# Optimization experiments

Measured on AMD Instinct MI355X. Metric: run time of the kernel, lower is better.

Reference implementation:

```python
import jax, jax.numpy as jnp
import numpy as np

B, C, H, W = 8, 128, 64, 64

def conv2d(x, w, b, pad):
    # x: [B,C,H,W], w: [O,I,kh,kw] -> NCHW conv with symmetric padding
    y = jax.lax.conv_general_dilated(
        x, w, window_strides=(1, 1), padding=[(pad, pad), (pad, pad)],
        dimension_numbers=("NCHW", "OIHW", "NCHW"))
    return y + b[None, :, None, None]

def setup_inputs() -> dict:
    key = jax.random.key(0)
    ks = jax.random.split(key, 5)
    s3 = 1.0 / np.sqrt(C * 9)  # kaiming-uniform-ish scale for 3x3 conv
    s1 = 1.0 / np.sqrt(C)
    return {
        "x": jax.random.normal(ks[0], (B, C, H, W), jnp.float32),
        "Wq": jax.random.normal(ks[1], (C, C, 3, 3), jnp.float32) * s3,
        "bq": jnp.zeros((C,), jnp.float32),
        "Wk": jax.random.normal(ks[2], (C, C, 3, 3), jnp.float32) * s3,
        "bk": jnp.zeros((C,), jnp.float32),
        "Wv": jax.random.normal(ks[3], (C, C, 3, 3), jnp.float32) * s3,
        "bv": jnp.zeros((C,), jnp.float32),
        "Wo": jax.random.normal(ks[4], (C, C, 1, 1), jnp.float32) * s1,
        "bo": jnp.zeros((C,), jnp.float32),
    }

def reference(x, Wq, bq, Wk, bk, Wv, bv, Wo, bo):
    b, c, h, w = x.shape
    n = h * w
    scale = c ** (-0.5)
    # NOTE: original module defines self.norm but never applies it in forward.
    q = conv2d(x, Wq, bq, 1).reshape(b, c, n)
    k = conv2d(x, Wk, bk, 1).reshape(b, c, n)
    v = conv2d(x, Wv, bv, 1).reshape(b, c, n)
    attn = jax.nn.softmax(jnp.einsum("bci,bcj->bij", q, k) * scale, axis=2)  # [b,n,n]
    out = jnp.einsum("bij,bcj->bci", attn, v).reshape(b, c, h, w)
    out = conv2d(out, Wo, bo, 0)
    return x + out
```

## Files before the change

kernel.cpp:

```cpp
#include <hip/hip_runtime.h>

typedef __attribute__((ext_vector_type(8))) short bf16x8;
typedef __attribute__((ext_vector_type(4))) float f32x4;
typedef __attribute__((ext_vector_type(16))) float f32x16;

static __device__ __forceinline__ unsigned short f2bf(float f) {
    union { float f; unsigned int u; } v; v.f = f;
    unsigned int r = v.u + 0x7FFFu + ((v.u >> 16) & 1u);
    return (unsigned short)(r >> 16);
}

static __device__ __forceinline__ unsigned cvtpk_bf16(float lo, float hi) {
    unsigned r;
    asm("v_cvt_pk_bf16_f32 %0, %1, %2" : "=v"(r) : "v"(lo), "v"(hi));
    return r;
}

#define NRW (27 * 16384)

__global__ __launch_bounds__(256) void repack_k(const float* __restrict__ Wq, const float* __restrict__ Wk,
                                                const float* __restrict__ Wv, const float* __restrict__ Wo,
                                                unsigned short* __restrict__ RW, unsigned short* __restrict__ WoB) {
    int t = blockIdx.x * 256 + threadIdx.x;
    if (t < NRW) {
        int s = t & 7, o = (t >> 3) & 127, g = (t >> 10) & 3, cc = (t >> 12) & 3, tap = t >> 14;
        int conv = tap / 9, kk = tap % 9, kh = kk / 3, kw = kk % 3;
        int c = cc * 32 + g * 8 + s;
        const float* W = (conv == 0) ? Wq : ((conv == 1) ? Wk : Wv);
        RW[t] = f2bf(W[((o * 128 + c) * 3 + kh) * 3 + kw]);
    } else {
        int u = t - NRW;
        if (u < 16384) WoB[u] = f2bf(Wo[u]);
    }
}

__global__ __launch_bounds__(256) void qkv_conv_k(const float* __restrict__ x, const unsigned short* __restrict__ RW,
                                                  const float* __restrict__ bq, const float* __restrict__ bk,
                                                  const float* __restrict__ bv,
                                                  unsigned short* __restrict__ q_ws, unsigned short* __restrict__ k_ws,
                                                  unsigned short* __restrict__ v_ws) {
    __shared__ unsigned short xs[3 * 66 * 128];
    const int tid = threadIdx.x;
    const int b = blockIdx.x >> 6, h = blockIdx.x & 63;
    for (int i = tid; i < 3 * 66 * 128; i += 256) xs[i] = 0;
    __syncthreads();
    for (int ch = tid; ch < 3 * 128 * 16; ch += 256) {
        int r3 = ch >> 11, rem = ch & 2047, c = rem >> 4, w4 = rem & 15;
        int hh = h - 1 + r3;
        if (hh >= 0 && hh < 64) {
            float4 v = *(const float4*)(x + ((b * 128 + c) * 64 + hh) * 64 + w4 * 4);
            float vv[4] = {v.x, v.y, v.z, v.w};
#pragma unroll
            for (int j = 0; j < 4; ++j) {
                int wr = w4 * 4 + j + 1;
                unsigned int byte = (unsigned int)(((r3 * 66 + wr) * 128 + c) * 2) ^ ((wr & 7) << 4);
                *(unsigned short*)((char*)xs + byte) = f2bf(vv[j]);
            }
        }
    }
    __syncthreads();
    const int lane = tid & 63, wave = tid >> 6;
    const int l15 = lane & 15, g = lane >> 4;
    f32x4 acc[4][6];
#pragma unroll
    for (int i = 0; i < 4; ++i)
#pragma unroll
        for (int j = 0; j < 6; ++j) acc[i][j] = (f32x4){0.f, 0.f, 0.f, 0.f};
#pragma unroll 1
    for (int kk = 0; kk < 9; ++kk) {
        const int kw = kk % 3;
#pragma unroll 2
        for (int cc = 0; cc < 4; ++cc) {
            bf16x8 a[4];
#pragma unroll
            for (int mf = 0; mf < 4; ++mf) {
                int wr = mf * 16 + l15 + kw;
                unsigned int byte = (unsigned int)((((kk / 3) * 66 + wr) * 128 + cc * 32 + g * 8) * 2) ^ ((wr & 7) << 4);
                a[mf] = *(const bf16x8*)((const char*)xs + byte);
            }
#pragma unroll
            for (int n6 = 0; n6 < 6; ++n6) {
                int nt = wave * 6 + n6;
                int conv = nt >> 3;
                int o = (nt * 16 + l15) & 127;
                bf16x8 bfr = *(const bf16x8*)(RW + ((((conv * 9 + kk) * 4 + cc) * 4 + g) * 128 + o) * 8);
#pragma unroll
                for (int mf = 0; mf < 4; ++mf)
                    acc[mf][n6] = __builtin_amdgcn_mfma_f32_16x16x32_bf16(a[mf], bfr, acc[mf][n6], 0, 0, 0);
            }
        }
    }
    const float SCALE = 0.08838834764831845f;
#pragma unroll
    for (int n6 = 0; n6 < 6; ++n6) {
        int nt = wave * 6 + n6;
        int conv = nt >> 3;
        int o = (nt * 16 + l15) & 127;
        float bias = (conv == 0) ? bq[o] : ((conv == 1) ? bk[o] : bv[o]);
#pragma unroll
        for (int mf = 0; mf < 4; ++mf) {
#pragma unroll
            for (int r = 0; r < 4; ++r) {
                int pos = h * 64 + mf * 16 + g * 4 + r;
                float val = acc[mf][n6][r] + bias;
                if (conv == 0)      q_ws[(b * 4096 + pos) * 128 + o] = f2bf(val * SCALE);
                else if (conv == 1) k_ws[(b * 4096 + pos) * 128 + o] = f2bf(val);
                else                v_ws[(b * 128 + o) * 4096 + pos] = f2bf(val);
            }
        }
    }
}

#define AS1C(p) ((const __attribute__((address_space(1))) void*)(p))
#define AS3(p)  ((__attribute__((address_space(3))) void*)(p))

__global__ __launch_bounds__(256, 2) void attn_k(
    const unsigned short* __restrict__ q_ws, const unsigned short* __restrict__ k_ws,
    const unsigned short* __restrict__ v_ws, const unsigned short* __restrict__ WoB,
    const float* __restrict__ bo, const float* __restrict__ x, float* __restrict__ out) {
    __shared__ __align__(16) char smem[66560];

    const int tid = threadIdx.x;
    const int lane = tid & 63, wave = tid >> 6;
    const int wj = wave & 1, wi = wave >> 1;
    const int l31 = lane & 31, h = lane >> 5;
    const int b = blockIdx.x & 7;
    const int qt = blockIdx.x >> 3;
    const int ibase = qt * 64;

    const char* kB = (const char*)(k_ws + (size_t)b * 4096 * 128);
    const char* vB = (const char*)(v_ws + (size_t)b * 128 * 4096);

    auto stage = [&](int buf, int kt) {
        char* Kn = smem + buf * 32768;
        char* Vn = Kn + 16384;
#pragma unroll
        for (int q = 0; q < 4; ++q) {
            int slot = (wave * 4 + q) * 64 + lane;
            int krow = slot >> 4, ks = slot & 15;
            int kcs = ks ^ (krow & 15);
            __builtin_amdgcn_global_load_lds(AS1C(kB + (size_t)(kt * 64 + krow) * 256 + kcs * 16),
                                             AS3(Kn + slot * 16), 16, 0, 0);
            int vrow = slot >> 3, vs = slot & 7;
            int vcs = vs ^ (vrow & 7);
            __builtin_amdgcn_global_load_lds(AS1C(vB + (size_t)vrow * 8192 + kt * 128 + vcs * 16),
                                             AS3(Vn + slot * 16), 16, 0, 0);
        }
    };

    stage(0, 0);

    bf16x8 qf[8];
    {
        const unsigned short* qrow = q_ws + ((size_t)b * 4096 + ibase + wi * 32 + l31) * 128;
#pragma unroll
        for (int cc = 0; cc < 8; ++cc) qf[cc] = *(const bf16x8*)(qrow + cc * 16 + h * 8);
    }

    f32x16 oac[4];
#pragma unroll
    for (int cf = 0; cf < 4; ++cf)
#pragma unroll
        for (int r = 0; r < 16; ++r) oac[cf][r] = 0.f;
    float m = -1e30f, ssum = 0.f;

    __syncthreads();

#pragma unroll 1
    for (int kt = 0; kt < 64; ++kt) {
        const int cur = kt & 1;
        const char* Kc = smem + cur * 32768;
        const char* Vc = Kc + 16384;
        if (kt < 63) stage(cur ^ 1, kt + 1);

        f32x16 st;
#pragma unroll
        for (int r = 0; r < 16; ++r) st[r] = 0.f;
        const int jrow = wj * 32 + l31;
        __builtin_amdgcn_s_setprio(1);
#pragma unroll
        for (int cc = 0; cc < 8; ++cc) {
            unsigned byte = (unsigned)(jrow * 256 + (((cc * 2 + h) ^ (jrow & 15)) << 4));
            bf16x8 kf = *(const bf16x8*)(Kc + byte);
            st = __builtin_amdgcn_mfma_f32_32x32x16_bf16(kf, qf[cc], st, 0, 0, 0);
        }
        __builtin_amdgcn_s_setprio(0);

        float tmax = st[0];
#pragma unroll
        for (int r = 1; r < 16; ++r) tmax = fmaxf(tmax, st[r]);
        tmax = fmaxf(tmax, __shfl_xor(tmax, 32));
        if (!__all(tmax <= m)) {
            float mnew = fmaxf(m, tmax);
            float corr = __expf(m - mnew);
            ssum *= corr;
#pragma unroll
            for (int cf = 0; cf < 4; ++cf)
#pragma unroll
                for (int r = 0; r < 16; ++r) oac[cf][r] *= corr;
            m = mnew;
        }

        float ps = 0.f;
        bf16x8 pa[2];
#pragma unroll
        for (int js = 0; js < 2; ++js) {
            float pA0 = __expf(st[8 * js + 0] - m);
            float pA1 = __expf(st[8 * js + 1] - m);
            float pA2 = __expf(st[8 * js + 2] - m);
            float pA3 = __expf(st[8 * js + 3] - m);
            float pB0 = __expf(st[8 * js + 4] - m);
            float pB1 = __expf(st[8 * js + 5] - m);
            float pB2 = __expf(st[8 * js + 6] - m);
            float pB3 = __expf(st[8 * js + 7] - m);
            ps += ((pA0 + pA1) + (pA2 + pA3)) + ((pB0 + pB1) + (pB2 + pB3));
            unsigned a0 = cvtpk_bf16(pA0, pA1), a1 = cvtpk_bf16(pA2, pA3);
            unsigned b0 = cvtpk_bf16(pB0, pB1), b1 = cvtpk_bf16(pB2, pB3);
            auto r0 = __builtin_amdgcn_permlane32_swap(a0, b0, false, false);
            auto r1 = __builtin_amdgcn_permlane32_swap(a1, b1, false, false);
            union { unsigned w[4]; bf16x8 v; } pu;
            pu.w[0] = r0[0];
            pu.w[1] = r1[0];
            pu.w[2] = r0[1];
            pu.w[3] = r1[1];
            pa[js] = pu.v;
        }
        ps += __shfl_xor(ps, 32);
        ssum += ps;

        __builtin_amdgcn_s_setprio(1);
#pragma unroll
        for (int js = 0; js < 2; ++js) {
            const int chunk = wj * 4 + js * 2 + h;
#pragma unroll
            for (int cf = 0; cf < 4; ++cf) {
                int crow = cf * 32 + l31;
                unsigned vbyte = (unsigned)(crow * 128 + ((chunk ^ (crow & 7)) << 4));
                bf16x8 va = *(const bf16x8*)(Vc + vbyte);
                oac[cf] = __builtin_amdgcn_mfma_f32_32x32x16_bf16(va, pa[js], oac[cf], 0, 0, 0);
            }
        }
        __builtin_amdgcn_s_setprio(0);
        __syncthreads();
    }

    float* sRed = (float*)(smem + 65536);
    const int it = wi * 32 + l31;
    if (h == 0) {
        sRed[(wj * 64 + it) * 2] = m;
        sRed[(wj * 64 + it) * 2 + 1] = ssum;
    }
    __syncthreads();
    float m1 = sRed[((wj ^ 1) * 64 + it) * 2];
    float s1 = sRed[((wj ^ 1) * 64 + it) * 2 + 1];
    float M = fmaxf(m, m1);
    float aS = __expf(m - M);
    float inv = 1.0f / (aS * ssum + __expf(m1 - M) * s1);

    char* sBig = smem + 32768;
    if (wj == 1) {
#pragma unroll
        for (int cf = 0; cf < 4; ++cf)
#pragma unroll
            for (int g = 0; g < 4; ++g) {
                int c = cf * 32 + g * 8 + 4 * h;
                f32x4 v4;
#pragma unroll
                for (int k = 0; k < 4; ++k) v4[k] = aS * oac[cf][4 * g + k];
                unsigned byte = (unsigned)(it * 512 + c * 4) ^ ((it & 7) << 4);
                *(f32x4*)(sBig + byte) = v4;
            }
    }
    __syncthreads();
    unsigned short* sOut = (unsigned short*)smem;
    if (wj == 0) {
#pragma unroll
        for (int cf = 0; cf < 4; ++cf)
#pragma unroll
            for (int g = 0; g < 4; ++g) {
                int c = cf * 32 + g * 8 + 4 * h;
                unsigned rbyte = (unsigned)(it * 512 + c * 4) ^ ((it & 7) << 4);
                f32x4 rd = *(const f32x4*)((const char*)sBig + rbyte);
                float u0 = (aS * oac[cf][4 * g + 0] + rd[0]) * inv;
                float u1 = (aS * oac[cf][4 * g + 1] + rd[1]) * inv;
                float u2 = (aS * oac[cf][4 * g + 2] + rd[2]) * inv;
                float u3 = (aS * oac[cf][4 * g + 3] + rd[3]) * inv;
                uint2 pk;
                pk.x = cvtpk_bf16(u0, u1);
                pk.y = cvtpk_bf16(u2, u3);
                unsigned wbyte = (unsigned)(it * 256 + c * 2) ^ ((it & 15) << 4);
                *(uint2*)((char*)sOut + wbyte) = pk;
            }
    }
    __syncthreads();

#pragma unroll
    for (int t = 0; t < 2; ++t) {
        int tt = wave * 2 + t;
        int of = tt >> 1, ifl = tt & 1;
        int ir = ifl * 32 + l31;
        f32x16 acc;
#pragma unroll
        for (int r = 0; r < 16; ++r) acc[r] = 0.f;
#pragma unroll
        for (int cc = 0; cc < 8; ++cc) {
            unsigned bbyte = (unsigned)(ir * 256 + cc * 32 + h * 16) ^ ((ir & 15) << 4);
            bf16x8 bfr = *(const bf16x8*)((const char*)sOut + bbyte);
            bf16x8 wa = *(const bf16x8*)(WoB + (of * 32 + l31) * 128 + cc * 16 + h * 8);
            acc = __builtin_amdgcn_mfma_f32_32x32x16_bf16(wa, bfr, acc, 0, 0, 0);
        }
        int iglob = ibase + ir;
#pragma unroll
        for (int r = 0; r < 16; ++r) {
            int o = of * 32 + (r & 3) + 8 * (r >> 2) + 4 * h;
            size_t gidx = ((size_t)b * 128 + o) * 4096 + iglob;
            out[gidx] = acc[r] + bo[o] + x[gidx];
        }
    }
}

extern "C" void kernel_launch(void* const* d_in, const int* in_sizes, int n_in,
                              void* d_out, int out_size, void* d_ws, size_t ws_size,
                              hipStream_t stream) {
    const float* x  = (const float*)d_in[0];
    const float* Wq = (const float*)d_in[1];
    const float* bq = (const float*)d_in[2];
    const float* Wk = (const float*)d_in[3];
    const float* bk = (const float*)d_in[4];
    const float* Wv = (const float*)d_in[5];
    const float* bv = (const float*)d_in[6];
    const float* Wo = (const float*)d_in[7];
    const float* bo = (const float*)d_in[8];
    char* ws = (char*)d_ws;
    unsigned short* q_ws = (unsigned short*)(ws);
    unsigned short* k_ws = (unsigned short*)(ws + 8388608);
    unsigned short* v_ws = (unsigned short*)(ws + 16777216);
    unsigned short* RW   = (unsigned short*)(ws + 25165824);
    unsigned short* WoB  = (unsigned short*)(ws + 26050560);
    float* out = (float*)d_out;

    hipLaunchKernelGGL(repack_k, dim3(1792), dim3(256), 0, stream, Wq, Wk, Wv, Wo, RW, WoB);
    hipLaunchKernelGGL(qkv_conv_k, dim3(512), dim3(256), 0, stream, x, RW, bq, bk, bv, q_ws, k_ws, v_ws);
    hipLaunchKernelGGL(attn_k, dim3(512), dim3(256), 0, stream, q_ws, k_ws, v_ws, WoB, bo, x, out);
}
```

Before: 162.8 us.

## Fold log2e into Q scale, lazy rescale, new V swizzle, interleave PV MFMAs

```diff
diff --git a/kernel.cpp b/kernel.cpp
--- a/kernel.cpp
+++ b/kernel.cpp
@@ -90,7 +90,7 @@
             }
         }
     }
-    const float SCALE = 0.08838834764831845f;
+    const float SCALE2 = 0.08838834764831845f * 1.4426950408889634f;
 #pragma unroll
     for (int n6 = 0; n6 < 6; ++n6) {
         int nt = wave * 6 + n6;
@@ -103,7 +103,7 @@
             for (int r = 0; r < 4; ++r) {
                 int pos = h * 64 + mf * 16 + g * 4 + r;
                 float val = acc[mf][n6][r] + bias;
-                if (conv == 0)      q_ws[(b * 4096 + pos) * 128 + o] = f2bf(val * SCALE);
+                if (conv == 0)      q_ws[(b * 4096 + pos) * 128 + o] = f2bf(val * SCALE2);
                 else if (conv == 1) k_ws[(b * 4096 + pos) * 128 + o] = f2bf(val);
                 else                v_ws[(b * 128 + o) * 4096 + pos] = f2bf(val);
             }
@@ -141,9 +141,10 @@
             int kcs = ks ^ (krow & 15);
             __builtin_amdgcn_global_load_lds(AS1C(kB + (size_t)(kt * 64 + krow) * 256 + kcs * 16),
                                              AS3(Kn + slot * 16), 16, 0, 0);
-            int vrow = slot >> 3, vs = slot & 7;
-            int vcs = vs ^ (vrow & 7);
-            __builtin_amdgcn_global_load_lds(AS1C(vB + (size_t)vrow * 8192 + kt * 128 + vcs * 16),
+            int sr = slot >> 4, s8p = slot & 15;
+            int s8 = s8p ^ (sr & 15);
+            int crow = sr * 2 + (s8 >> 3), jch = s8 & 7;
+            __builtin_amdgcn_global_load_lds(AS1C(vB + (size_t)crow * 8192 + kt * 128 + jch * 16),
                                              AS3(Vn + slot * 16), 16, 0, 0);
         }
     };
@@ -157,6 +158,9 @@
         for (int cc = 0; cc < 8; ++cc) qf[cc] = *(const bf16x8*)(qrow + cc * 16 + h * 8);
     }
 
+    f32x16 zero16;
+#pragma unroll
+    for (int r = 0; r < 16; ++r) zero16[r] = 0.f;
     f32x16 oac[4];
 #pragma unroll
     for (int cf = 0; cf < 4; ++cf)
@@ -173,26 +177,34 @@
         const char* Vc = Kc + 16384;
         if (kt < 63) stage(cur ^ 1, kt + 1);
 
+        const int jrow = wj * 32 + l31;
         f32x16 st;
-#pragma unroll
-        for (int r = 0; r < 16; ++r) st[r] = 0.f;
-        const int jrow = wj * 32 + l31;
         __builtin_amdgcn_s_setprio(1);
-#pragma unroll
-        for (int cc = 0; cc < 8; ++cc) {
+        {
+            unsigned byte = (unsigned)(jrow * 256 + ((h ^ (jrow & 15)) << 4));
+            bf16x8 kf = *(const bf16x8*)(Kc + byte);
+            st = __builtin_amdgcn_mfma_f32_32x32x16_bf16(kf, qf[0], zero16, 0, 0, 0);
+        }
+#pragma unroll
+        for (int cc = 1; cc < 8; ++cc) {
             unsigned byte = (unsigned)(jrow * 256 + (((cc * 2 + h) ^ (jrow & 15)) << 4));
             bf16x8 kf = *(const bf16x8*)(Kc + byte);
             st = __builtin_amdgcn_mfma_f32_32x32x16_bf16(kf, qf[cc], st, 0, 0, 0);
         }
         __builtin_amdgcn_s_setprio(0);
 
-        float tmax = st[0];
-#pragma unroll
-        for (int r = 1; r < 16; ++r) tmax = fmaxf(tmax, st[r]);
+        float x0 = fmaxf(fmaxf(st[0], st[1]), st[2]);
+        float x1 = fmaxf(fmaxf(st[3], st[4]), st[5]);
+        float x2 = fmaxf(fmaxf(st[6], st[7]), st[8]);
+        float x3 = fmaxf(fmaxf(st[9], st[10]), st[11]);
+        float x4 = fmaxf(fmaxf(st[12], st[13]), st[14]);
+        float y0 = fmaxf(fmaxf(x0, x1), x2);
+        float y1 = fmaxf(fmaxf(x3, x4), st[15]);
+        float tmax = fmaxf(y0, y1);
         tmax = fmaxf(tmax, __shfl_xor(tmax, 32));
-        if (!__all(tmax <= m)) {
+        if (!__all(tmax <= m + 8.f)) {
             float mnew = fmaxf(m, tmax);
-            float corr = __expf(m - mnew);
+            float corr = exp2f(m - mnew);
             ssum *= corr;
 #pragma unroll
             for (int cf = 0; cf < 4; ++cf)
@@ -202,17 +214,16 @@
         }
 
         float ps = 0.f;
-        bf16x8 pa[2];
 #pragma unroll
         for (int js = 0; js < 2; ++js) {
-            float pA0 = __expf(st[8 * js + 0] - m);
-            float pA1 = __expf(st[8 * js + 1] - m);
-            float pA2 = __expf(st[8 * js + 2] - m);
-            float pA3 = __expf(st[8 * js + 3] - m);
-            float pB0 = __expf(st[8 * js + 4] - m);
-            float pB1 = __expf(st[8 * js + 5] - m);
-            float pB2 = __expf(st[8 * js + 6] - m);
-            float pB3 = __expf(st[8 * js + 7] - m);
+            float pA0 = exp2f(st[8 * js + 0] - m);
+            float pA1 = exp2f(st[8 * js + 1] - m);
+            float pA2 = exp2f(st[8 * js + 2] - m);
+            float pA3 = exp2f(st[8 * js + 3] - m);
+            float pB0 = exp2f(st[8 * js + 4] - m);
+            float pB1 = exp2f(st[8 * js + 5] - m);
+            float pB2 = exp2f(st[8 * js + 6] - m);
+            float pB3 = exp2f(st[8 * js + 7] - m);
             ps += ((pA0 + pA1) + (pA2 + pA3)) + ((pB0 + pB1) + (pB2 + pB3));
             unsigned a0 = cvtpk_bf16(pA0, pA1), a1 = cvtpk_bf16(pA2, pA3);
             unsigned b0 = cvtpk_bf16(pB0, pB1), b1 = cvtpk_bf16(pB2, pB3);
@@ -223,24 +234,21 @@
             pu.w[1] = r1[0];
             pu.w[2] = r0[1];
             pu.w[3] = r1[1];
-            pa[js] = pu.v;
+            const int jch = wj * 4 + js * 2 + h;
+            __builtin_amdgcn_s_setprio(1);
+#pragma unroll
+            for (int cf = 0; cf < 4; ++cf) {
+                int crow = cf * 32 + l31;
+                int sr = crow >> 1;
+                int s8 = ((crow & 1) << 3) | jch;
+                unsigned vbyte = (unsigned)(sr * 256 + ((s8 ^ (sr & 15)) << 4));
+                bf16x8 va = *(const bf16x8*)(Vc + vbyte);
+                oac[cf] = __builtin_amdgcn_mfma_f32_32x32x16_bf16(va, pu.v, oac[cf], 0, 0, 0);
+            }
+            __builtin_amdgcn_s_setprio(0);
         }
         ps += __shfl_xor(ps, 32);
         ssum += ps;
-
-        __builtin_amdgcn_s_setprio(1);
-#pragma unroll
-        for (int js = 0; js < 2; ++js) {
-            const int chunk = wj * 4 + js * 2 + h;
-#pragma unroll
-            for (int cf = 0; cf < 4; ++cf) {
-                int crow = cf * 32 + l31;
-                unsigned vbyte = (unsigned)(crow * 128 + ((chunk ^ (crow & 7)) << 4));
-                bf16x8 va = *(const bf16x8*)(Vc + vbyte);
-                oac[cf] = __builtin_amdgcn_mfma_f32_32x32x16_bf16(va, pa[js], oac[cf], 0, 0, 0);
-            }
-        }
-        __builtin_amdgcn_s_setprio(0);
         __syncthreads();
     }
 
@@ -254,8 +262,8 @@
     float m1 = sRed[((wj ^ 1) * 64 + it) * 2];
     float s1 = sRed[((wj ^ 1) * 64 + it) * 2 + 1];
     float M = fmaxf(m, m1);
-    float aS = __expf(m - M);
-    float inv = 1.0f / (aS * ssum + __expf(m1 - M) * s1);
+    float aS = exp2f(m - M);
+    float inv = 1.0f / (aS * ssum + exp2f(m1 - M) * s1);
 
     char* sBig = smem + 32768;
     if (wj == 1) {
```

Measured after the change: 165.3 us. Within noise of the previous version (+1.5%).
